# Performance work log

Hardware: AMD Instinct MI355X
Metric: run time of the kernel (lower is better)

Reference implementation:

```python
import jax, jax.numpy as jnp
from jax import lax
import numpy as np
import math

B, T, HID = 4, 2048, 1024
NH, KS, INTER = 8, 4, 2816
HD = HID // NH
CHUNK = 32
EPS = 1e-6


def setup_inputs() -> dict:
    key = jax.random.key(0)
    ks = jax.random.split(key, 16)
    def w(k, shape, fan_in):
        return jax.random.normal(k, shape, jnp.float32) * (1.0 / math.sqrt(fan_in))
    logit = math.log(0.95 / 0.05)
    return {
        'x': jax.random.normal(ks[0], (B, T, HID), jnp.float32),
        'qkv_w': w(ks[1], (3 * HID, HID), HID),
        'out_proj_w': w(ks[2], (HID, HID), HID),
        'out_gate_w': w(ks[3], (HID, HID), HID),
        'out_gate_b': jnp.zeros((HID,), jnp.float32),
        'decay_param': jnp.full((NH,), logit, jnp.float32),
        'conv_w': w(ks[4], (HID, 1, KS), KS),      # depthwise: [out, in/groups=1, k]
        'conv_b': jnp.zeros((HID,), jnp.float32),
        'pw_w': w(ks[5], (HID, HID), HID),
        'gate_w': w(ks[6], (HID, 2 * HID), 2 * HID),
        'w1': w(ks[7], (INTER, HID), HID),
        'w2': w(ks[8], (INTER, HID), HID),
        'w3': w(ks[9], (HID, INTER), INTER),
        'norm1_w': jnp.ones((HID,), jnp.float32),
        'norm2_w': jnp.ones((HID,), jnp.float32),
    }


def rmsnorm(x, w, eps=EPS):
    ms = jnp.mean(jnp.square(x), axis=-1, keepdims=True)
    return x * lax.rsqrt(ms + eps) * w


def decay_scan(x, decay, init):
    # inclusive scan out[t] = decay*out[t-1] + x[t]; x:[B,NH,T,HD], decay:[1,NH,1], init:[B,NH,HD]
    b, h, t, d = x.shape
    c = min(CHUNK, t)
    log_d = jnp.log(jnp.maximum(decay.astype(jnp.float32), 1e-8))        # [1,NH,1]
    idx = jnp.arange(c, dtype=jnp.float32)
    log_p = log_d[..., None] * idx[None, None, :, None]                  # [1,NH,c,1]
    p, inv_p = jnp.exp(log_p), jnp.exp(-log_p)
    init_p = jnp.exp(log_d[..., None] * (idx + 1.0)[None, None, :, None])
    xc = x.astype(jnp.float32).reshape(b, h, t // c, c, d)
    xc = jnp.moveaxis(xc, 2, 0)                                          # [Nc,B,NH,c,HD]
    def step(state, chunk):
        cs = jnp.cumsum(chunk * inv_p, axis=2)
        out = cs * p + state[:, :, None, :] * init_p
        return out[:, :, -1, :], out
    _, outs = lax.scan(step, init.astype(jnp.float32), xc)
    out = jnp.moveaxis(outs, 0, 2).reshape(b, h, t, d)
    return out.astype(x.dtype)


def _forward(x, qkv_w, out_proj_w, out_gate_w, out_gate_b, decay_param,
             conv_w, conv_b, pw_w, gate_w, w1, w2, w3, norm1_w, norm2_w):
    b, t, _ = x.shape
    h = rmsnorm(x, norm1_w)

    # ---- LocalConv (depthwise causal conv + pointwise) ----
    xc = jnp.transpose(h, (0, 2, 1))                                     # [B,HID,T]
    pad = jnp.zeros((b, HID, KS - 1), x.dtype)
    xc = jnp.concatenate([pad, xc], axis=2)
    conv = lax.conv_general_dilated(xc, conv_w, (1,), 'VALID',
                                    dimension_numbers=('NCH', 'OIH', 'NCH'),
                                    feature_group_count=HID)
    conv = conv + conv_b[None, :, None]
    conv = jnp.transpose(conv, (0, 2, 1))                                # [B,T,HID]
    local = jnp.einsum('bth,oh->bto', jax.nn.silu(conv), pw_w)

    # ---- LinearAttention ----
    qkv = jnp.einsum('bth,oh->bto', h, qkv_w)
    q, k, v = jnp.split(qkv, 3, axis=-1)
    def heads(z):
        return jnp.transpose(z.reshape(b, t, NH, HD), (0, 2, 1, 3))      # [B,NH,T,HD]
    q, k, v = heads(q), heads(k), heads(v)
    q = jax.nn.elu(q) + 1.0
    k = jax.nn.elu(k) + 1.0
    decay = jax.nn.sigmoid(decay_param).reshape(1, NH, 1)
    zero_state = jnp.zeros((b, NH, HD), x.dtype)
    running_kv = decay_scan(k * v, decay, zero_state)
    running_ks = decay_scan(k, decay, zero_state)
    den = jnp.maximum(jnp.sum(q * running_ks, axis=-1, keepdims=True), 1e-6)
    o = q * running_kv / den                                             # [B,NH,T,HD]
    v_direct = jnp.transpose(v, (0, 2, 1, 3)).reshape(b, t, HID)
    o = jnp.transpose(o, (0, 2, 1, 3)).reshape(b, t, HID)
    g = jax.nn.sigmoid(jnp.einsum('bth,oh->bto', o, out_gate_w) + out_gate_b)
    o = g * o + (1.0 - g) * v_direct
    attn = jnp.einsum('bth,oh->bto', o, out_proj_w)

    # ---- Gate fusion of local/global, residual ----
    comb = jnp.concatenate([local, attn], axis=-1)
    gmix = jax.nn.sigmoid(jnp.einsum('bth,oh->bto', comb, gate_w))
    x = x + gmix * local + (1.0 - gmix) * attn

    # ---- FFN (SwiGLU) + residual ----
    h2 = rmsnorm(x, norm2_w)
    ffn = jnp.einsum('bti,oi->bto',
                     jax.nn.silu(jnp.einsum('bth,ih->bti', h2, w1)) *
                     jnp.einsum('bth,ih->bti', h2, w2), w3)
    return x + ffn


def reference(x, qkv_w, out_proj_w, out_gate_w, out_gate_b, decay_param,
              conv_w, conv_b, pw_w, gate_w, w1, w2, w3, norm1_w, norm2_w):
    return _forward(x, qkv_w, out_proj_w, out_gate_w, out_gate_b, decay_param,
                    conv_w, conv_b, pw_w, gate_w, w1, w2, w3, norm1_w, norm2_w)
```

## Files before the change

### kernel.cpp

```cpp
#include <hip/hip_runtime.h>
#include <math.h>

static constexpr int Bc    = 4;
static constexpr int Tc    = 2048;
static constexpr int HIDc  = 1024;
static constexpr int NHc   = 8;
static constexpr int HDc   = 128;
static constexpr int Mrows = Bc * Tc;
static constexpr int INTERc= 2816;
static constexpr int CH    = 64;
static constexpr int NC    = Tc / CH;

typedef _Float16 f16;
typedef __attribute__((ext_vector_type(8))) _Float16 f16x8;
typedef __attribute__((ext_vector_type(4))) float f32x4;
typedef unsigned short u16;

union H8 { f16 h[8]; int4 v; u16 u[8]; };
union H4 { f16 h[4]; int2 v; u16 u[4]; };
union F4 { float4 v; float a[4]; };

static __device__ __forceinline__ float sigm(float x) { return 1.0f / (1.0f + expf(-x)); }
static __device__ __forceinline__ float silu(float x) { return x * sigm(x); }
static __device__ __forceinline__ float elu1(float x) { return x > 0.0f ? x + 1.0f : expf(x); }

static __device__ __forceinline__ float h2f(u16 u){ f16 h; __builtin_memcpy(&h,&u,2); return (float)h; }
static __device__ __forceinline__ u16 f2h(float x){ f16 h=(f16)x; u16 u; __builtin_memcpy(&u,&h,2); return u; }
static __device__ __forceinline__ float rec2(u16 h, u16 l){ return h2f(h) + h2f(l); }
static __device__ __forceinline__ void fsplit(float v, u16& h, u16& l){ h = f2h(v); l = f2h(v - h2f(h)); }

__global__ __launch_bounds__(256) void wcvt_k(const float* __restrict__ src,
                                              u16* __restrict__ dst, int n8)
{
    const int i = blockIdx.x * 256 + threadIdx.x;
    if (i >= n8) return;
    F4 a, b; a.v = ((const float4*)src)[i * 2]; b.v = ((const float4*)src)[i * 2 + 1];
    H8 o;
    #pragma unroll
    for (int u = 0; u < 4; u++) { o.h[u] = (f16)a.a[u]; o.h[4 + u] = (f16)b.a[u]; }
    ((int4*)dst)[i] = o.v;
}

template<int INPAIR>
__global__ __launch_bounds__(256) void rmsnorm_k(const float* __restrict__ xf,
                                                 const u16* __restrict__ xhi,
                                                 const u16* __restrict__ xlo,
                                                 const float* __restrict__ w,
                                                 u16* __restrict__ ohi,
                                                 u16* __restrict__ olo)
{
    const int row = blockIdx.x;
    const int tid = threadIdx.x;
    const size_t off = (size_t)row * HIDc + tid * 4;
    float xv[4];
    if constexpr (INPAIR) {
        H4 H, L;
        H.v = *(const int2*)(xhi + off);
        L.v = *(const int2*)(xlo + off);
        #pragma unroll
        for (int u = 0; u < 4; u++) xv[u] = (float)H.h[u] + (float)L.h[u];
    } else {
        F4 f; f.v = *(const float4*)(xf + off);
        #pragma unroll
        for (int u = 0; u < 4; u++) xv[u] = f.a[u];
    }
    float ss = xv[0]*xv[0] + xv[1]*xv[1] + xv[2]*xv[2] + xv[3]*xv[3];
    #pragma unroll
    for (int o = 32; o > 0; o >>= 1) ss += __shfl_xor(ss, o);
    __shared__ float sred[4];
    if ((tid & 63) == 0) sred[tid >> 6] = ss;
    __syncthreads();
    const float tot = sred[0] + sred[1] + sred[2] + sred[3];
    const float scale = rsqrtf(tot * (1.0f / (float)HIDc) + 1e-6f);
    F4 wv; wv.v = *(const float4*)(w + tid * 4);
    H4 OH, OL;
    #pragma unroll
    for (int u = 0; u < 4; u++) {
        u16 hh, ll; fsplit(xv[u] * scale * wv.a[u], hh, ll);
        OH.u[u] = hh; OL.u[u] = ll;
    }
    *(int2*)(ohi + off) = OH.v;
    *(int2*)(olo + off) = OL.v;
}

__global__ __launch_bounds__(256) void conv_k(const u16* __restrict__ hhi,
                                              const u16* __restrict__ hlo,
                                              const float* __restrict__ cw,
                                              const float* __restrict__ cb,
                                              u16* __restrict__ ohi,
                                              u16* __restrict__ olo)
{
    const int row = blockIdx.x;
    const int t   = row & (Tc - 1);
    const int ch4 = threadIdx.x * 4;
    const float* wp = cw + (size_t)ch4 * 4;
    F4 bias; bias.v = *(const float4*)(cb + ch4);
    F4 acc;
    #pragma unroll
    for (int u = 0; u < 4; u++) acc.a[u] = bias.a[u];
    #pragma unroll
    for (int j = 0; j < 4; j++) {
        const int tt = t - 3 + j;
        if (tt >= 0) {
            const size_t off = ((size_t)row + j - 3) * HIDc + ch4;
            H4 H, L;
            H.v = *(const int2*)(hhi + off);
            L.v = *(const int2*)(hlo + off);
            #pragma unroll
            for (int u = 0; u < 4; u++) acc.a[u] += ((float)H.h[u] + (float)L.h[u]) * wp[u * 4 + j];
        }
    }
    H4 OH, OL;
    #pragma unroll
    for (int u = 0; u < 4; u++) {
        u16 hh, ll; fsplit(silu(acc.a[u]), hh, ll);
        OH.u[u] = hh; OL.u[u] = ll;
    }
    const size_t off = (size_t)row * HIDc + ch4;
    *(int2*)(ohi + off) = OH.v;
    *(int2*)(olo + off) = OL.v;
}

__global__ __launch_bounds__(64) void scan1_k(u16* __restrict__ khi, u16* __restrict__ klo,
                                              const u16* __restrict__ vhi, const u16* __restrict__ vlo,
                                              u16* __restrict__ shi, u16* __restrict__ slo,
                                              const float* __restrict__ dp)
{
    const int bid = blockIdx.x;
    const int c   = bid & (NC - 1);
    const int bh  = bid >> 5;
    const int b   = bh >> 3, hh = bh & 7;
    const int lane = threadIdx.x;
    const float dec = sigm(dp[hh]);
    const size_t base = (size_t)b * Tc * HIDc + (size_t)(c * CH) * HIDc + hh * HDc + lane * 2;
    float skv0 = 0.f, skv1 = 0.f, sks0 = 0.f, sks1 = 0.f;
    for (int t = 0; t < CH; t++) {
        const size_t p = base + (size_t)t * HIDc;
        const unsigned kh = *(const unsigned*)(khi + p);
        const unsigned kl = *(const unsigned*)(klo + p);
        const unsigned vh = *(const unsigned*)(vhi + p);
        const unsigned vl = *(const unsigned*)(vlo + p);
        const float kx = elu1(rec2((u16)kh, (u16)kl));
        const float ky = elu1(rec2((u16)(kh >> 16), (u16)(kl >> 16)));
        const float vx = rec2((u16)vh, (u16)vl);
        const float vy = rec2((u16)(vh >> 16), (u16)(vl >> 16));
        skv0 = dec * skv0 + kx * vx;
        skv1 = dec * skv1 + ky * vy;
        sks0 = dec * sks0 + kx;
        sks1 = dec * sks1 + ky;
        u16 h0, l0, h1, l1;
        fsplit(skv0, h0, l0); fsplit(skv1, h1, l1);
        *(unsigned*)(khi + p) = (unsigned)h0 | ((unsigned)h1 << 16);
        *(unsigned*)(klo + p) = (unsigned)l0 | ((unsigned)l1 << 16);
        fsplit(sks0, h0, l0); fsplit(sks1, h1, l1);
        *(unsigned*)(shi + p) = (unsigned)h0 | ((unsigned)h1 << 16);
        *(unsigned*)(slo + p) = (unsigned)l0 | ((unsigned)l1 << 16);
    }
}

__global__ __launch_bounds__(64) void scan2_k(u16* __restrict__ qhi, u16* __restrict__ qlo,
                                              const u16* __restrict__ skvhi, const u16* __restrict__ skvlo,
                                              const u16* __restrict__ skshi, const u16* __restrict__ skslo,
                                              const float* __restrict__ dp)
{
    const int bid = blockIdx.x;
    const int c   = bid & (NC - 1);
    const int bh  = bid >> 5;
    const int b   = bh >> 3, hh = bh & 7;
    const int lane = threadIdx.x;
    const float dec = sigm(dp[hh]);
    float dCH = dec;
    #pragma unroll
    for (int i = 0; i < 6; i++) dCH *= dCH;
    const size_t rowbase = (size_t)b * Tc * HIDc + hh * HDc + lane * 2;

    float ckv0 = 0.f, ckv1 = 0.f, cks0 = 0.f, cks1 = 0.f;
    for (int j = 0; j < c; j++) {
        const size_t p = rowbase + (size_t)(j * CH + CH - 1) * HIDc;
        const unsigned ah = *(const unsigned*)(skvhi + p);
        const unsigned al = *(const unsigned*)(skvlo + p);
        const unsigned bh2 = *(const unsigned*)(skshi + p);
        const unsigned bl2 = *(const unsigned*)(skslo + p);
        ckv0 = ckv0 * dCH + rec2((u16)ah, (u16)al);
        ckv1 = ckv1 * dCH + rec2((u16)(ah >> 16), (u16)(al >> 16));
        cks0 = cks0 * dCH + rec2((u16)bh2, (u16)bl2);
        cks1 = cks1 * dCH + rec2((u16)(bh2 >> 16), (u16)(bl2 >> 16));
    }

    const size_t cbase = rowbase + (size_t)(c * CH) * HIDc;
    float pw = dec;
    for (int t = 0; t < CH; t++) {
        const size_t p = cbase + (size_t)t * HIDc;
        const unsigned qh = *(const unsigned*)(qhi + p);
        const unsigned ql = *(const unsigned*)(qlo + p);
        const unsigned ah = *(const unsigned*)(skvhi + p);
        const unsigned al = *(const unsigned*)(skvlo + p);
        const unsigned bh2 = *(const unsigned*)(skshi + p);
        const unsigned bl2 = *(const unsigned*)(skslo + p);
        const float qx = elu1(rec2((u16)qh, (u16)ql));
        const float qy = elu1(rec2((u16)(qh >> 16), (u16)(ql >> 16)));
        const float skv0 = rec2((u16)ah, (u16)al) + pw * ckv0;
        const float skv1 = rec2((u16)(ah >> 16), (u16)(al >> 16)) + pw * ckv1;
        const float sks0 = rec2((u16)bh2, (u16)bl2) + pw * cks0;
        const float sks1 = rec2((u16)(bh2 >> 16), (u16)(bl2 >> 16)) + pw * cks1;
        float part = qx * sks0 + qy * sks1;
        #pragma unroll
        for (int o = 32; o > 0; o >>= 1) part += __shfl_xor(part, o);
        const float inv = 1.0f / fmaxf(part, 1e-6f);
        u16 h0, l0, h1, l1;
        fsplit(qx * skv0 * inv, h0, l0);
        fsplit(qy * skv1 * inv, h1, l1);
        *(unsigned*)(qhi + p) = (unsigned)h0 | ((unsigned)h1 << 16);
        *(unsigned*)(qlo + p) = (unsigned)l0 | ((unsigned)l1 << 16);
        pw *= dec;
    }
}

template<int MODE, int PRE>
__global__ __launch_bounds__(256) void gemm_f16_k(
    const u16* __restrict__ Ahi, const u16* __restrict__ Alo,
    const u16* __restrict__ A2hi, const u16* __restrict__ A2lo, int lda,
    const u16* __restrict__ Wh, const float* __restrict__ Wf,
    float* __restrict__ Cout,
    u16* __restrict__ Chi, u16* __restrict__ Clo, int ldc,
    int K, int kSplit, const float* __restrict__ bias,
    const float* __restrict__ E0f,
    const u16* __restrict__ E0hi, const u16* __restrict__ E0lo, int ldE0,
    const u16* __restrict__ E1hi, const u16* __restrict__ E1lo, int ldE1,
    const u16* __restrict__ E2hi, const u16* __restrict__ E2lo, int ldE2)
{
    __shared__ __align__(16) u16 Ah[4][129][8];
    __shared__ __align__(16) u16 Al[4][129][8];
    __shared__ __align__(16) u16 Bs[4][129][8];

    const int tid  = threadIdx.x;
    const int lane = tid & 63;
    const int w    = tid >> 6;
    const int wr   = w >> 1, wc = w & 1;
    const int lr   = lane & 15, lk = lane >> 4;
    const int m0 = blockIdx.y * 128, n0 = blockIdx.x * 128;

    const int arow = tid & 127;
    const int ksel = tid >> 7;
    const int cA   = ksel * 2;

    f32x4 acc[4][4];
    #pragma unroll
    for (int i = 0; i < 4; i++)
        #pragma unroll
        for (int j = 0; j < 4; j++)
            acc[i][j] = (f32x4){0.f, 0.f, 0.f, 0.f};

    for (int k0 = 0; k0 < K; k0 += 32) {
        const u16* ah = Ahi; const u16* al = Alo; int kb = k0;
        if constexpr (MODE == 4) {
            if (k0 >= kSplit) { ah = A2hi; al = A2lo; kb = k0 - kSplit; }
        }
        const size_t aoff = (size_t)(m0 + arow) * lda + kb + ksel * 16;
        const int4 a0 = *(const int4*)(ah + aoff);
        const int4 a1 = *(const int4*)(ah + aoff + 8);
        const int4 l0 = *(const int4*)(al + aoff);
        const int4 l1 = *(const int4*)(al + aoff + 8);
        int4 w0, w1;
        if constexpr (PRE) {
            const size_t woff = (size_t)(n0 + arow) * K + k0 + ksel * 16;
            w0 = *(const int4*)(Wh + woff);
            w1 = *(const int4*)(Wh + woff + 8);
        } else {
            const float* wpf = Wf + (size_t)(n0 + arow) * K + k0 + ksel * 16;
            F4 g[4];
            #pragma unroll
            for (int q = 0; q < 4; q++) g[q].v = *(const float4*)(wpf + q * 4);
            H8 W0, W1;
            #pragma unroll
            for (int e = 0; e < 8; e++) {
                W0.h[e] = (f16)g[e >> 2].a[e & 3];
                W1.h[e] = (f16)g[2 + (e >> 2)].a[e & 3];
            }
            w0 = W0.v; w1 = W1.v;
        }
        __syncthreads();
        *(int4*)&Ah[cA][arow][0]     = a0;
        *(int4*)&Ah[cA + 1][arow][0] = a1;
        *(int4*)&Al[cA][arow][0]     = l0;
        *(int4*)&Al[cA + 1][arow][0] = l1;
        *(int4*)&Bs[cA][arow][0]     = w0;
        *(int4*)&Bs[cA + 1][arow][0] = w1;
        __syncthreads();
        f16x8 av[4], au[4], bv[4];
        #pragma unroll
        for (int fi = 0; fi < 4; fi++) {
            av[fi] = *(const f16x8*)&Ah[lk][wr * 64 + fi * 16 + lr][0];
            au[fi] = *(const f16x8*)&Al[lk][wr * 64 + fi * 16 + lr][0];
            bv[fi] = *(const f16x8*)&Bs[lk][wc * 64 + fi * 16 + lr][0];
        }
        #pragma unroll
        for (int i = 0; i < 4; i++)
            #pragma unroll
            for (int j = 0; j < 4; j++) {
                acc[i][j] = __builtin_amdgcn_mfma_f32_16x16x32_f16(av[i], bv[j], acc[i][j], 0, 0, 0);
                acc[i][j] = __builtin_amdgcn_mfma_f32_16x16x32_f16(au[i], bv[j], acc[i][j], 0, 0, 0);
            }
    }

    #pragma unroll
    for (int i = 0; i < 4; i++) {
        #pragma unroll
        for (int j = 0; j < 4; j++) {
            #pragma unroll
            for (int v = 0; v < 4; v++) {
                const size_t r = (size_t)(m0 + wr * 64 + i * 16 + lk * 4 + v);
                const int c = n0 + wc * 64 + j * 16 + lr;
                const size_t idx = r * (size_t)ldc + c;
                float val = acc[i][j][v];
                if constexpr (MODE == 1) {
                    val = silu(val);
                } else if constexpr (MODE == 2) {
                    val = rec2(Chi[idx], Clo[idx]) * val;
                } else if constexpr (MODE == 3) {
                    const float g = sigm(val + bias[c]);
                    const size_t i0 = r * (size_t)ldE0 + c, i1 = r * (size_t)ldE1 + c;
                    val = g * rec2(E0hi[i0], E0lo[i0]) + (1.0f - g) * rec2(E1hi[i1], E1lo[i1]);
                } else if constexpr (MODE == 4) {
                    const float g = sigm(val);
                    const size_t i1 = r * (size_t)ldE1 + c, i2 = r * (size_t)ldE2 + c;
                    val = E0f[r * (size_t)ldE0 + c] + g * rec2(E1hi[i1], E1lo[i1])
                          + (1.0f - g) * rec2(E2hi[i2], E2lo[i2]);
                } else if constexpr (MODE == 6) {
                    Cout[idx] = rec2(Chi[idx], Clo[idx]) + val;
                    continue;
                }
                u16 hh, ll; fsplit(val, hh, ll);
                Chi[idx] = hh; Clo[idx] = ll;
            }
        }
    }
}

template<int MODE>
static inline void launch_gemm(bool pre, dim3 grid, hipStream_t stream,
    const u16* Ahi, const u16* Alo, const u16* A2hi, const u16* A2lo, int lda,
    const u16* Wh, const float* Wf,
    float* Cout, u16* Chi, u16* Clo, int ldc, int K, int kSplit,
    const float* bias, const float* E0f,
    const u16* E0hi, const u16* E0lo, int ldE0,
    const u16* E1hi, const u16* E1lo, int ldE1,
    const u16* E2hi, const u16* E2lo, int ldE2)
{
    if (pre)
        gemm_f16_k<MODE, 1><<<grid, dim3(256), 0, stream>>>(Ahi, Alo, A2hi, A2lo, lda, Wh, Wf,
            Cout, Chi, Clo, ldc, K, kSplit, bias, E0f, E0hi, E0lo, ldE0, E1hi, E1lo, ldE1, E2hi, E2lo, ldE2);
    else
        gemm_f16_k<MODE, 0><<<grid, dim3(256), 0, stream>>>(Ahi, Alo, A2hi, A2lo, lda, Wh, Wf,
            Cout, Chi, Clo, ldc, K, kSplit, bias, E0f, E0hi, E0lo, ldE0, E1hi, E1lo, ldE1, E2hi, E2lo, ldE2);
}

extern "C" void kernel_launch(void* const* d_in, const int* in_sizes, int n_in,
                              void* d_out, int out_size, void* d_ws, size_t ws_size,
                              hipStream_t stream)
{
    const float* x           = (const float*)d_in[0];
    const float* qkv_w       = (const float*)d_in[1];
    const float* out_proj_w  = (const float*)d_in[2];
    const float* out_gate_w  = (const float*)d_in[3];
    const float* out_gate_b  = (const float*)d_in[4];
    const float* decay_param = (const float*)d_in[5];
    const float* conv_w      = (const float*)d_in[6];
    const float* conv_b      = (const float*)d_in[7];
    const float* pw_w        = (const float*)d_in[8];
    const float* gate_w      = (const float*)d_in[9];
    const float* w1          = (const float*)d_in[10];
    const float* w2          = (const float*)d_in[11];
    const float* w3          = (const float*)d_in[12];
    const float* norm1_w     = (const float*)d_in[13];
    const float* norm2_w     = (const float*)d_in[14];
    float* OUT = (float*)d_out;

    float* ws = (float*)d_ws;
    const size_t S8 = (size_t)Mrows * HIDc;
    u16* P0h = (u16*)(ws + 0 * S8); u16* P0l = P0h + S8;
    u16* P1h = (u16*)(ws + 1 * S8); u16* P1l = P1h + S8;
    u16* P2h = (u16*)(ws + 2 * S8); u16* P2l = P2h + S8;
    u16* P3h = (u16*)(ws + 3 * S8); u16* P3l = P3h + S8;
    u16* OUTh = (u16*)OUT;          u16* OUTl = OUTh + S8;
    u16* T1h = P1h;                 u16* T1l = P1h + (size_t)Mrows * INTERc;

    constexpr size_t SZ_QKV  = (size_t)3 * HIDc * HIDc;
    constexpr size_t SZ_SQ   = (size_t)HIDc * HIDc;
    constexpr size_t SZ_GATE = (size_t)2 * HIDc * HIDc;
    constexpr size_t SZ_W1   = (size_t)INTERc * HIDc;
    constexpr size_t W_ELEMS = SZ_QKV + 3 * SZ_SQ + SZ_GATE + 3 * SZ_W1;
    const bool pre = (ws_size >= 4 * S8 * sizeof(float) + W_ELEMS * sizeof(u16));

    u16* wb   = (u16*)(ws + 4 * S8);
    u16* qkvH = wb;
    u16* pwH  = qkvH + SZ_QKV;
    u16* ogH  = pwH  + SZ_SQ;
    u16* opH  = ogH  + SZ_SQ;
    u16* gaH  = opH  + SZ_SQ;
    u16* w1H  = gaH  + SZ_GATE;
    u16* w2H  = w1H  + SZ_W1;
    u16* w3H  = w2H  + SZ_W1;

    const dim3 blk(256);
    const dim3 g8(8, Mrows / 128);
    const dim3 g22(22, Mrows / 128);
    const u16* nu = nullptr;

    if (pre) {
        wcvt_k<<<(int)(SZ_QKV / 8 / 256), blk, 0, stream>>>(qkv_w, qkvH, (int)(SZ_QKV / 8));
        wcvt_k<<<(int)(SZ_SQ  / 8 / 256), blk, 0, stream>>>(pw_w,  pwH,  (int)(SZ_SQ  / 8));
        wcvt_k<<<(int)(SZ_SQ  / 8 / 256), blk, 0, stream>>>(out_gate_w, ogH, (int)(SZ_SQ / 8));
        wcvt_k<<<(int)(SZ_SQ  / 8 / 256), blk, 0, stream>>>(out_proj_w, opH, (int)(SZ_SQ / 8));
        wcvt_k<<<(int)(SZ_GATE/ 8 / 256), blk, 0, stream>>>(gate_w, gaH, (int)(SZ_GATE / 8));
        wcvt_k<<<(int)(SZ_W1  / 8 / 256), blk, 0, stream>>>(w1, w1H, (int)(SZ_W1 / 8));
        wcvt_k<<<(int)(SZ_W1  / 8 / 256), blk, 0, stream>>>(w2, w2H, (int)(SZ_W1 / 8));
        wcvt_k<<<(int)(SZ_W1  / 8 / 256), blk, 0, stream>>>(w3, w3H, (int)(SZ_W1 / 8));
    }

    rmsnorm_k<0><<<Mrows, blk, 0, stream>>>(x, nullptr, nullptr, norm1_w, P0h, P0l);
    conv_k<<<Mrows, blk, 0, stream>>>(P0h, P0l, conv_w, conv_b, P1h, P1l);
    launch_gemm<0>(pre, g8, stream, P1h, P1l, nu, nu, HIDc, pwH, pw_w,
                   nullptr, P2h, P2l, HIDc, HIDc, 0, nullptr, nullptr,
                   nu, nu, 0, nu, nu, 0, nu, nu, 0);
    launch_gemm<0>(pre, g8, stream, P0h, P0l, nu, nu, HIDc, qkvH, qkv_w,
                   nullptr, P1h, P1l, HIDc, HIDc, 0, nullptr, nullptr,
                   nu, nu, 0, nu, nu, 0, nu, nu, 0);
    launch_gemm<0>(pre, g8, stream, P0h, P0l, nu, nu, HIDc, qkvH + SZ_SQ, qkv_w + SZ_SQ,
                   nullptr, P3h, P3l, HIDc, HIDc, 0, nullptr, nullptr,
                   nu, nu, 0, nu, nu, 0, nu, nu, 0);
    launch_gemm<0>(pre, g8, stream, P0h, P0l, nu, nu, HIDc, qkvH + 2 * SZ_SQ, qkv_w + 2 * SZ_SQ,
                   nullptr, OUTh, OUTl, HIDc, HIDc, 0, nullptr, nullptr,
                   nu, nu, 0, nu, nu, 0, nu, nu, 0);
    scan1_k<<<Bc * NHc * NC, dim3(64), 0, stream>>>(P3h, P3l, OUTh, OUTl, P0h, P0l, decay_param);
    scan2_k<<<Bc * NHc * NC, dim3(64), 0, stream>>>(P1h, P1l, P3h, P3l, P0h, P0l, decay_param);
    launch_gemm<3>(pre, g8, stream, P1h, P1l, nu, nu, HIDc, ogH, out_gate_w,
                   nullptr, P0h, P0l, HIDc, HIDc, 0, out_gate_b, nullptr,
                   P1h, P1l, HIDc, OUTh, OUTl, HIDc, nu, nu, 0);
    launch_gemm<0>(pre, g8, stream, P0h, P0l, nu, nu, HIDc, opH, out_proj_w,
                   nullptr, P3h, P3l, HIDc, HIDc, 0, nullptr, nullptr,
                   nu, nu, 0, nu, nu, 0, nu, nu, 0);
    launch_gemm<4>(pre, g8, stream, P2h, P2l, P3h, P3l, HIDc, gaH, gate_w,
                   nullptr, P0h, P0l, HIDc, 2 * HIDc, HIDc, nullptr, x,
                   nu, nu, HIDc, P2h, P2l, HIDc, P3h, P3l, HIDc);
    rmsnorm_k<1><<<Mrows, blk, 0, stream>>>(nullptr, P0h, P0l, norm2_w, OUTh, OUTl);
    launch_gemm<1>(pre, g22, stream, OUTh, OUTl, nu, nu, HIDc, w1H, w1,
                   nullptr, T1h, T1l, INTERc, HIDc, 0, nullptr, nullptr,
                   nu, nu, 0, nu, nu, 0, nu, nu, 0);
    launch_gemm<2>(pre, g22, stream, OUTh, OUTl, nu, nu, HIDc, w2H, w2,
                   nullptr, T1h, T1l, INTERc, HIDc, 0, nullptr, nullptr,
                   nu, nu, 0, nu, nu, 0, nu, nu, 0);
    launch_gemm<6>(pre, g8, stream, T1h, T1l, nu, nu, INTERc, w3H, w3,
                   OUT, P0h, P0l, HIDc, INTERc, 0, nullptr, nullptr,
                   nu, nu, 0, nu, nu, 0, nu, nu, 0);
}
```

Baseline: 1.403 ms.

## Load GEMM tiles straight into LDS and remap block IDs across XCDs

The GEMM tile loads of A hi/lo and the pre-converted weights now use global_load_lds, which writes global data directly into shared memory instead of staging it through registers. The LDS tiles lose their padding row, and the thread-to-row mapping changes so each wave fills one k-slice for 64 consecutive rows. The grid becomes 1D with a block-ID swizzle (bid&7)*cpx + bid>>3, so blocks that land on the same XCD work on adjacent tiles and share L2. Dropping the padding can cause LDS bank conflicts when the MFMA fragments are read.

```diff
diff --git a/kernel.cpp b/kernel.cpp
--- a/kernel.cpp
+++ b/kernel.cpp
@@ -28,6 +28,13 @@
 static __device__ __forceinline__ u16 f2h(float x){ f16 h=(f16)x; u16 u; __builtin_memcpy(&u,&h,2); return u; }
 static __device__ __forceinline__ float rec2(u16 h, u16 l){ return h2f(h) + h2f(l); }
 static __device__ __forceinline__ void fsplit(float v, u16& h, u16& l){ h = f2h(v); l = f2h(v - h2f(h)); }
+
+static __device__ __forceinline__ void gld16(const u16* g, u16* l)
+{
+    __builtin_amdgcn_global_load_lds((const __attribute__((address_space(1))) void*)g,
+                                     (__attribute__((address_space(3))) void*)l,
+                                     16, 0, 0);
+}
 
 __global__ __launch_bounds__(256) void wcvt_k(const float* __restrict__ src,
                                               u16* __restrict__ dst, int n8)
@@ -223,26 +230,28 @@
     const u16* __restrict__ Wh, const float* __restrict__ Wf,
     float* __restrict__ Cout,
     u16* __restrict__ Chi, u16* __restrict__ Clo, int ldc,
-    int K, int kSplit, const float* __restrict__ bias,
+    int K, int kSplit, int nx,
+    const float* __restrict__ bias,
     const float* __restrict__ E0f,
     const u16* __restrict__ E0hi, const u16* __restrict__ E0lo, int ldE0,
     const u16* __restrict__ E1hi, const u16* __restrict__ E1lo, int ldE1,
     const u16* __restrict__ E2hi, const u16* __restrict__ E2lo, int ldE2)
 {
-    __shared__ __align__(16) u16 Ah[4][129][8];
-    __shared__ __align__(16) u16 Al[4][129][8];
-    __shared__ __align__(16) u16 Bs[4][129][8];
+    __shared__ __align__(16) u16 Ah[4][128][8];
+    __shared__ __align__(16) u16 Al[4][128][8];
+    __shared__ __align__(16) u16 Bs[4][128][8];
 
     const int tid  = threadIdx.x;
     const int lane = tid & 63;
-    const int w    = tid >> 6;
-    const int wr   = w >> 1, wc = w & 1;
+    const int wv   = tid >> 6;
+    const int wr   = wv >> 1, wc = wv & 1;
     const int lr   = lane & 15, lk = lane >> 4;
-    const int m0 = blockIdx.y * 128, n0 = blockIdx.x * 128;
-
-    const int arow = tid & 127;
-    const int ksel = tid >> 7;
-    const int cA   = ksel * 2;
+
+    const int cpx = gridDim.x >> 3;
+    int bid = blockIdx.x;
+    bid = (bid & 7) * cpx + (bid >> 3);
+    const int n0 = (bid % nx) * 128;
+    const int m0 = (bid / nx) * 128;
 
     f32x4 acc[4][4];
     #pragma unroll
@@ -256,36 +265,39 @@
         if constexpr (MODE == 4) {
             if (k0 >= kSplit) { ah = A2hi; al = A2lo; kb = k0 - kSplit; }
         }
-        const size_t aoff = (size_t)(m0 + arow) * lda + kb + ksel * 16;
-        const int4 a0 = *(const int4*)(ah + aoff);
-        const int4 a1 = *(const int4*)(ah + aoff + 8);
-        const int4 l0 = *(const int4*)(al + aoff);
-        const int4 l1 = *(const int4*)(al + aoff + 8);
-        int4 w0, w1;
+        const size_t a0off = (size_t)(m0 + lane) * lda + kb + wv * 8;
+        const size_t a1off = a0off + (size_t)64 * lda;
+        F4 wreg[4];
+        size_t w0off = 0, w1off = 0;
         if constexpr (PRE) {
-            const size_t woff = (size_t)(n0 + arow) * K + k0 + ksel * 16;
-            w0 = *(const int4*)(Wh + woff);
-            w1 = *(const int4*)(Wh + woff + 8);
+            w0off = (size_t)(n0 + lane) * K + k0 + wv * 8;
+            w1off = w0off + (size_t)64 * K;
         } else {
-            const float* wpf = Wf + (size_t)(n0 + arow) * K + k0 + ksel * 16;
-            F4 g[4];
-            #pragma unroll
-            for (int q = 0; q < 4; q++) g[q].v = *(const float4*)(wpf + q * 4);
+            const float* wp0 = Wf + (size_t)(n0 + lane) * K + k0 + wv * 8;
+            const float* wp1 = wp0 + (size_t)64 * K;
+            wreg[0].v = *(const float4*)(wp0);
+            wreg[1].v = *(const float4*)(wp0 + 4);
+            wreg[2].v = *(const float4*)(wp1);
+            wreg[3].v = *(const float4*)(wp1 + 4);
+        }
+        __syncthreads();
+        gld16(ah + a0off, &Ah[wv][0][0]);
+        gld16(ah + a1off, &Ah[wv][64][0]);
+        gld16(al + a0off, &Al[wv][0][0]);
+        gld16(al + a1off, &Al[wv][64][0]);
+        if constexpr (PRE) {
+            gld16(Wh + w0off, &Bs[wv][0][0]);
+            gld16(Wh + w1off, &Bs[wv][64][0]);
+        } else {
             H8 W0, W1;
             #pragma unroll
             for (int e = 0; e < 8; e++) {
-                W0.h[e] = (f16)g[e >> 2].a[e & 3];
-                W1.h[e] = (f16)g[2 + (e >> 2)].a[e & 3];
+                W0.h[e] = (f16)wreg[e >> 2].a[e & 3];
+                W1.h[e] = (f16)wreg[2 + (e >> 2)].a[e & 3];
             }
-            w0 = W0.v; w1 = W1.v;
-        }
-        __syncthreads();
-        *(int4*)&Ah[cA][arow][0]     = a0;
-        *(int4*)&Ah[cA + 1][arow][0] = a1;
-        *(int4*)&Al[cA][arow][0]     = l0;
-        *(int4*)&Al[cA + 1][arow][0] = l1;
-        *(int4*)&Bs[cA][arow][0]     = w0;
-        *(int4*)&Bs[cA + 1][arow][0] = w1;
+            *(int4*)&Bs[wv][lane][0]      = W0.v;
+            *(int4*)&Bs[wv][64 + lane][0] = W1.v;
+        }
         __syncthreads();
         f16x8 av[4], au[4], bv[4];
         #pragma unroll
@@ -338,7 +350,7 @@
 }
 
 template<int MODE>
-static inline void launch_gemm(bool pre, dim3 grid, hipStream_t stream,
+static inline void launch_gemm(bool pre, int nblocks, int nx, hipStream_t stream,
     const u16* Ahi, const u16* Alo, const u16* A2hi, const u16* A2lo, int lda,
     const u16* Wh, const float* Wf,
     float* Cout, u16* Chi, u16* Clo, int ldc, int K, int kSplit,
@@ -348,11 +360,11 @@
     const u16* E2hi, const u16* E2lo, int ldE2)
 {
     if (pre)
-        gemm_f16_k<MODE, 1><<<grid, dim3(256), 0, stream>>>(Ahi, Alo, A2hi, A2lo, lda, Wh, Wf,
-            Cout, Chi, Clo, ldc, K, kSplit, bias, E0f, E0hi, E0lo, ldE0, E1hi, E1lo, ldE1, E2hi, E2lo, ldE2);
+        gemm_f16_k<MODE, 1><<<dim3(nblocks), dim3(256), 0, stream>>>(Ahi, Alo, A2hi, A2lo, lda, Wh, Wf,
+            Cout, Chi, Clo, ldc, K, kSplit, nx, bias, E0f, E0hi, E0lo, ldE0, E1hi, E1lo, ldE1, E2hi, E2lo, ldE2);
     else
-        gemm_f16_k<MODE, 0><<<grid, dim3(256), 0, stream>>>(Ahi, Alo, A2hi, A2lo, lda, Wh, Wf,
-            Cout, Chi, Clo, ldc, K, kSplit, bias, E0f, E0hi, E0lo, ldE0, E1hi, E1lo, ldE1, E2hi, E2lo, ldE2);
+        gemm_f16_k<MODE, 0><<<dim3(nblocks), dim3(256), 0, stream>>>(Ahi, Alo, A2hi, A2lo, lda, Wh, Wf,
+            Cout, Chi, Clo, ldc, K, kSplit, nx, bias, E0f, E0hi, E0lo, ldE0, E1hi, E1lo, ldE1, E2hi, E2lo, ldE2);
 }
 
 extern "C" void kernel_launch(void* const* d_in, const int* in_sizes, int n_in,
@@ -403,8 +415,8 @@
     u16* w3H  = w2H  + SZ_W1;
 
     const dim3 blk(256);
-    const dim3 g8(8, Mrows / 128);
-    const dim3 g22(22, Mrows / 128);
+    const int nb8  = 8 * (Mrows / 128);
+    const int nb22 = 22 * (Mrows / 128);
     const u16* nu = nullptr;
 
     if (pre) {
@@ -420,37 +432,37 @@
 
     rmsnorm_k<0><<<Mrows, blk, 0, stream>>>(x, nullptr, nullptr, norm1_w, P0h, P0l);
     conv_k<<<Mrows, blk, 0, stream>>>(P0h, P0l, conv_w, conv_b, P1h, P1l);
-    launch_gemm<0>(pre, g8, stream, P1h, P1l, nu, nu, HIDc, pwH, pw_w,
+    launch_gemm<0>(pre, nb8, 8, stream, P1h, P1l, nu, nu, HIDc, pwH, pw_w,
                    nullptr, P2h, P2l, HIDc, HIDc, 0, nullptr, nullptr,
                    nu, nu, 0, nu, nu, 0, nu, nu, 0);
-    launch_gemm<0>(pre, g8, stream, P0h, P0l, nu, nu, HIDc, qkvH, qkv_w,
+    launch_gemm<0>(pre, nb8, 8, stream, P0h, P0l, nu, nu, HIDc, qkvH, qkv_w,
                    nullptr, P1h, P1l, HIDc, HIDc, 0, nullptr, nullptr,
                    nu, nu, 0, nu, nu, 0, nu, nu, 0);
-    launch_gemm<0>(pre, g8, stream, P0h, P0l, nu, nu, HIDc, qkvH + SZ_SQ, qkv_w + SZ_SQ,
+    launch_gemm<0>(pre, nb8, 8, stream, P0h, P0l, nu, nu, HIDc, qkvH + SZ_SQ, qkv_w + SZ_SQ,
                    nullptr, P3h, P3l, HIDc, HIDc, 0, nullptr, nullptr,
                    nu, nu, 0, nu, nu, 0, nu, nu, 0);
-    launch_gemm<0>(pre, g8, stream, P0h, P0l, nu, nu, HIDc, qkvH + 2 * SZ_SQ, qkv_w + 2 * SZ_SQ,
+    launch_gemm<0>(pre, nb8, 8, stream, P0h, P0l, nu, nu, HIDc, qkvH + 2 * SZ_SQ, qkv_w + 2 * SZ_SQ,
                    nullptr, OUTh, OUTl, HIDc, HIDc, 0, nullptr, nullptr,
                    nu, nu, 0, nu, nu, 0, nu, nu, 0);
     scan1_k<<<Bc * NHc * NC, dim3(64), 0, stream>>>(P3h, P3l, OUTh, OUTl, P0h, P0l, decay_param);
     scan2_k<<<Bc * NHc * NC, dim3(64), 0, stream>>>(P1h, P1l, P3h, P3l, P0h, P0l, decay_param);
-    launch_gemm<3>(pre, g8, stream, P1h, P1l, nu, nu, HIDc, ogH, out_gate_w,
+    launch_gemm<3>(pre, nb8, 8, stream, P1h, P1l, nu, nu, HIDc, ogH, out_gate_w,
                    nullptr, P0h, P0l, HIDc, HIDc, 0, out_gate_b, nullptr,
                    P1h, P1l, HIDc, OUTh, OUTl, HIDc, nu, nu, 0);
-    launch_gemm<0>(pre, g8, stream, P0h, P0l, nu, nu, HIDc, opH, out_proj_w,
+    launch_gemm<0>(pre, nb8, 8, stream, P0h, P0l, nu, nu, HIDc, opH, out_proj_w,
                    nullptr, P3h, P3l, HIDc, HIDc, 0, nullptr, nullptr,
                    nu, nu, 0, nu, nu, 0, nu, nu, 0);
-    launch_gemm<4>(pre, g8, stream, P2h, P2l, P3h, P3l, HIDc, gaH, gate_w,
+    launch_gemm<4>(pre, nb8, 8, stream, P2h, P2l, P3h, P3l, HIDc, gaH, gate_w,
                    nullptr, P0h, P0l, HIDc, 2 * HIDc, HIDc, nullptr, x,
                    nu, nu, HIDc, P2h, P2l, HIDc, P3h, P3l, HIDc);
     rmsnorm_k<1><<<Mrows, blk, 0, stream>>>(nullptr, P0h, P0l, norm2_w, OUTh, OUTl);
-    launch_gemm<1>(pre, g22, stream, OUTh, OUTl, nu, nu, HIDc, w1H, w1,
+    launch_gemm<1>(pre, nb22, 22, stream, OUTh, OUTl, nu, nu, HIDc, w1H, w1,
                    nullptr, T1h, T1l, INTERc, HIDc, 0, nullptr, nullptr,
                    nu, nu, 0, nu, nu, 0, nu, nu, 0);
-    launch_gemm<2>(pre, g22, stream, OUTh, OUTl, nu, nu, HIDc, w2H, w2,
+    launch_gemm<2>(pre, nb22, 22, stream, OUTh, OUTl, nu, nu, HIDc, w2H, w2,
                    nullptr, T1h, T1l, INTERc, HIDc, 0, nullptr, nullptr,
                    nu, nu, 0, nu, nu, 0, nu, nu, 0);
-    launch_gemm<6>(pre, g8, stream, T1h, T1l, nu, nu, INTERc, w3H, w3,
+    launch_gemm<6>(pre, nb8, 8, stream, T1h, T1l, nu, nu, INTERc, w3H, w3,
                    OUT, P0h, P0l, HIDc, INTERc, 0, nullptr, nullptr,
                    nu, nu, 0, nu, nu, 0, nu, nu, 0);
 }
```

Measured after the change: 1.285 ms. 8.4% less time.
